# Optimization experiments

Hardware: AMD Instinct MI355X
Metric: run time of the kernel (lower is better)

## Reference

```python
import jax, jax.numpy as jnp
import numpy as np

B, S, H = 64, 512, 1024  # batch, seq_len, hidden (input_size == hidden_size per source)


def setup_inputs() -> dict:
    key = jax.random.key(0)
    k1, k2 = jax.random.split(key)
    x = jax.random.normal(k1, (B, S, H), dtype=jnp.float32)
    # xavier_uniform_ for U: bound = sqrt(6/(fan_in+fan_out))
    bound = float(np.sqrt(6.0 / (H + 4 * H)))
    U = jax.random.uniform(k2, (H, 4 * H), dtype=jnp.float32, minval=-bound, maxval=bound)
    bias = jnp.zeros((4 * H,), dtype=jnp.float32)
    return {"x": x, "U": U, "bias": bias}


def reference(x, U, bias):
    # Faithful LSTM recurrence (peephole=False; note: W is declared in the
    # original module but never used in forward, and the gate matmul uses U
    # on the input x_t, exactly as in the source).
    batch = x.shape[0]
    HS = U.shape[0]
    h0 = jnp.zeros((batch, HS), dtype=x.dtype)
    c0 = jnp.zeros((batch, HS), dtype=x.dtype)

    def step(carry, x_t):
        h_t, c_t = carry
        gates = x_t @ U + bias  # [B, 4H]
        i_t = jax.nn.sigmoid(gates[:, :HS])
        f_t = jax.nn.sigmoid(gates[:, HS:2 * HS])
        g_t = jnp.tanh(gates[:, 2 * HS:3 * HS])
        o_t = jax.nn.sigmoid(gates[:, 3 * HS:])
        c_t = f_t * c_t + i_t * g_t
        h_t = o_t * jnp.tanh(c_t)
        return (h_t, c_t), h_t

    (h_T, c_T), hs = jax.lax.scan(step, (h0, c0), jnp.swapaxes(x, 0, 1))  # hs: [S, B, H]
    hidden_sequence = jnp.swapaxes(hs, 0, 1)  # [B, S, H]
    return hidden_sequence, (h_T, c_T)
```

## Files before the change

### kernel.cpp

```cpp
#include <hip/hip_runtime.h>
#include <hip/hip_bf16.h>
#include <stdint.h>

typedef __bf16 bf16x8 __attribute__((ext_vector_type(8)));
typedef float  f32x4  __attribute__((ext_vector_type(4)));
typedef unsigned short u16x8 __attribute__((ext_vector_type(8)));
typedef unsigned short u16x4 __attribute__((ext_vector_type(4)));
typedef _Float16 f16x4 __attribute__((ext_vector_type(4)));

#define HS    1024
#define FOURH 4096
#define SEQ   512
#define BATCH 64

#define BAR()  asm volatile("s_barrier" ::: "memory")
#define VMW(n) asm volatile("s_waitcnt vmcnt(" #n ")" ::: "memory")

__device__ __forceinline__ unsigned short f2bf(float f) {
    unsigned u = __builtin_bit_cast(unsigned, f);
    u = (u + 0x7FFFu + ((u >> 16) & 1u)) >> 16;
    return (unsigned short)u;
}

__device__ __forceinline__ void gload_lds16(const void* g, void* l) {
    __builtin_amdgcn_global_load_lds(
        (const __attribute__((address_space(1))) void*)g,
        (__attribute__((address_space(3))) void*)l, 16, 0, 0);
}

__device__ __forceinline__ float fsigmoid(float v) {
    return __builtin_amdgcn_rcpf(1.f + __expf(-v));
}
__device__ __forceinline__ float ftanh(float v) {
    return 1.f - 2.f * __builtin_amdgcn_rcpf(1.f + __expf(2.f * v));
}

__global__ __launch_bounds__(256) void convert_x(const float* __restrict__ x,
                                                 unsigned short* __restrict__ xb,
                                                 long n8) {
    long i = (long)blockIdx.x * blockDim.x + threadIdx.x;
    long stride = (long)gridDim.x * blockDim.x;
    for (; i < n8; i += stride) {
        const float4* p = (const float4*)(x + i * 8);
        float4 a = p[0], b = p[1];
        u16x8 o;
        o[0] = f2bf(a.x); o[1] = f2bf(a.y); o[2] = f2bf(a.z); o[3] = f2bf(a.w);
        o[4] = f2bf(b.x); o[5] = f2bf(b.y); o[6] = f2bf(b.z); o[7] = f2bf(b.w);
        *(u16x8*)(xb + i * 8) = o;
    }
}

__global__ __launch_bounds__(256) void transpose_u(const float* __restrict__ U,
                                                   unsigned short* __restrict__ Ut) {
    __shared__ float tile[32][33];
    int bx = blockIdx.x;
    int tn = bx >> 5;
    int tk = bx & 31;
    int c = threadIdx.x & 31;
    int r = threadIdx.x >> 5;
#pragma unroll
    for (int i = 0; i < 4; ++i) {
        int k = tk * 32 + r + i * 8;
        tile[r + i * 8][c] = U[(size_t)k * FOURH + tn * 32 + c];
    }
    __syncthreads();
#pragma unroll
    for (int i = 0; i < 4; ++i) {
        int nl = r + i * 8;
        Ut[(size_t)(tn * 32 + nl) * HS + tk * 32 + c] = f2bf(tile[c][nl]);
    }
}

__global__ __launch_bounds__(512, 1) void gemm_gates8(
    const unsigned short* __restrict__ Xb,
    const unsigned short* __restrict__ Ut,
    const float* __restrict__ bias,
    _Float16* __restrict__ gates,
    int lg2chunk, int s0) {
    __shared__ unsigned short LDSU[65536];

    int nwg = gridDim.x;
    int bid = blockIdx.x;
    int wg = (bid & 7) * (nwg >> 3) + (bid >> 3);
    int mt = wg >> 4;
    int nt = wg & 15;

    int tid = threadIdx.x;
    int w = tid >> 6, l = tid & 63;
    int wr = w >> 2, wc = w & 3;
    int lr = l & 15, lg = l >> 4;

    const int m0 = mt * 256, n0 = nt * 256;
    const int cmask = (1 << lg2chunk) - 1;

    const int rdo = lr * 32 + ((lg * 8) ^ ((lr & 8) << 1));

    const int srow = l >> 2;
    const int skin = ((l & 3) * 8) ^ (((l >> 5) & 1) << 4);

    const unsigned short* pAq[4];
    const unsigned short* pBq[4];
#pragma unroll
    for (int q = 0; q < 4; ++q) {
        int rowg = q * 64 + (w >> 1) * 16 + srow;
        int mrow = m0 + rowg;
        int b = mrow >> lg2chunk, sl2 = mrow & cmask;
        pAq[q] = Xb + (size_t)(b * SEQ + s0 + sl2) * HS + (w & 1) * 32 + skin;
        pBq[q] = Ut + (size_t)(n0 + rowg) * HS + (w & 1) * 32 + skin;
    }
    const int dsub = (w >> 1) * 2 + (w & 1);

    f32x4 acc[8][4];
#pragma unroll
    for (int mi = 0; mi < 8; ++mi)
#pragma unroll
        for (int ni = 0; ni < 4; ++ni) acc[mi][ni] = 0.f;

#define SA(T, Q) gload_lds16(pAq[Q] + (T) * 64, \
        &LDSU[(((T) & 1) << 15) + ((Q) * 8 + dsub) * 512])
#define SB(T, Q) gload_lds16(pBq[Q] + (T) * 64, \
        &LDSU[(((T) & 1) << 15) + 16384 + ((Q) * 8 + dsub) * 512])

    bf16x8 aq[2][4], bn0[2][2], bn1[2][2];

#define RDA(MH) \
    _Pragma("unroll") for (int ks = 0; ks < 2; ++ks) \
    _Pragma("unroll") for (int mi = 0; mi < 4; ++mi) \
        aq[ks][mi] = *(const bf16x8*)(buf + ((wr * 8 + (MH) * 4 + mi) * 2 + ks) * 512 + rdo)
#define RDB(NH, BN) \
    _Pragma("unroll") for (int ks = 0; ks < 2; ++ks) \
    _Pragma("unroll") for (int ni = 0; ni < 2; ++ni) \
        BN[ks][ni] = *(const bf16x8*)(buf + 16384 + ((wc * 4 + (NH) * 2 + ni) * 2 + ks) * 512 + rdo)
#define MMQ(MH, NH, BN) \
    __builtin_amdgcn_s_setprio(1); \
    _Pragma("unroll") for (int ks = 0; ks < 2; ++ks) \
    _Pragma("unroll") for (int mi = 0; mi < 4; ++mi) \
    _Pragma("unroll") for (int ni = 0; ni < 2; ++ni) \
        acc[(MH) * 4 + mi][(NH) * 2 + ni] = __builtin_amdgcn_mfma_f32_16x16x32_bf16( \
            aq[ks][mi], BN[ks][ni], acc[(MH) * 4 + mi][(NH) * 2 + ni], 0, 0, 0); \
    __builtin_amdgcn_s_setprio(0)

    SA(0, 0); SA(0, 2); SB(0, 0); SB(0, 1); SB(0, 2); SB(0, 3); SA(0, 1); SA(0, 3);
    VMW(2); BAR();

    for (int t = 0; t < 16; ++t) {
        const unsigned short* buf = &LDSU[(t & 1) << 15];
        RDA(0);
        RDB(0, bn0);
        if (t < 15) { SA(t + 1, 0); SA(t + 1, 2); }
        MMQ(0, 0, bn0);
        RDB(1, bn1);
        if (t < 15) { SB(t + 1, 0); SB(t + 1, 1); SB(t + 1, 2); SB(t + 1, 3); }
        MMQ(0, 1, bn1);
        if (t < 15) { VMW(6); } else { VMW(0); }
        BAR();
        RDA(1);
        if (t < 15) { SA(t + 1, 1); SA(t + 1, 3); }
        MMQ(1, 1, bn1);
        MMQ(1, 0, bn0);
        if (t < 15) { VMW(2); }
        BAR();
    }

#pragma unroll
    for (int ni = 0; ni < 4; ++ni) {
        int gcol = n0 + wc * 64 + ni * 16 + lr;
        bool is_g = ((gcol >> 10) == 2);
        float bv = bias[gcol];
#pragma unroll
        for (int mi = 0; mi < 8; ++mi) {
            int rg = ((m0 + wr * 128 + mi * 16) >> 2) + lg;
            u16x4 pk;
#pragma unroll
            for (int r = 0; r < 4; ++r) {
                float v = acc[mi][ni][r] + bv;
                float e = is_g ? ftanh(v) : fsigmoid(v);
                pk[r] = __builtin_bit_cast(unsigned short, (_Float16)e);
            }
            *(u16x4*)(gates + ((size_t)rg * FOURH + gcol) * 4) = pk;
        }
    }
#undef SA
#undef SB
#undef RDA
#undef RDB
#undef MMQ
}

__global__ __launch_bounds__(256) void lstm_recur(
    const _Float16* __restrict__ gates,
    float* __restrict__ out,
    float* __restrict__ cstate,
    int chunk, int s0) {
    int t = blockIdx.x * 256 + threadIdx.x;
    int b = t >> 10, h = t & 1023;
    float c = (s0 == 0) ? 0.f : cstate[t];
    const _Float16* gp = gates + ((size_t)((b * chunk) >> 2) * FOURH + h) * 4;
    float* op = out + (size_t)(b * SEQ + s0) * HS + h;
    float hv = 0.f;
    const int ng = chunk >> 2;
    for (int g4 = 0; g4 < ng; g4 += 2) {
        f16x4 iv[2], fv[2], gv[2], ov[2];
#pragma unroll
        for (int u = 0; u < 2; ++u) {
            const _Float16* q = gp + (size_t)(g4 + u) * (FOURH * 4);
            iv[u] = *(const f16x4*)(q);
            fv[u] = *(const f16x4*)(q + 4096);
            gv[u] = *(const f16x4*)(q + 8192);
            ov[u] = *(const f16x4*)(q + 12288);
        }
#pragma unroll
        for (int u = 0; u < 2; ++u) {
#pragma unroll
            for (int r = 0; r < 4; ++r) {
                c = (float)fv[u][r] * c + (float)iv[u][r] * (float)gv[u][r];
                float th = ftanh(c);
                hv = (float)ov[u][r] * th;
                op[(size_t)((g4 + u) * 4 + r) * HS] = hv;
            }
        }
    }
    cstate[t] = c;
    if (s0 + chunk == SEQ) {
        out[(size_t)BATCH * SEQ * HS + t] = hv;
        out[(size_t)BATCH * SEQ * HS + BATCH * HS + t] = c;
    }
}

extern "C" void kernel_launch(void* const* d_in, const int* in_sizes, int n_in,
                              void* d_out, int out_size, void* d_ws, size_t ws_size,
                              hipStream_t stream) {
    const float* x    = (const float*)d_in[0];
    const float* U    = (const float*)d_in[1];
    const float* bias = (const float*)d_in[2];
    float* out = (float*)d_out;
    char*  ws  = (char*)d_ws;

    unsigned short* Xb = (unsigned short*)ws;
    unsigned short* Ut = (unsigned short*)(ws + 67108864);
    float* cstate      = (float*)(ws + 75497472);
    _Float16* gates    = (_Float16*)(ws + 75759616);
    const size_t fixed = 75759616;

    int chunk = 512;
    while (chunk > 4 && fixed + (size_t)BATCH * chunk * FOURH * 2 > ws_size)
        chunk >>= 1;
    int lg2 = 31 - __builtin_clz(chunk);

    convert_x<<<2048, 256, 0, stream>>>(x, Xb, (long)BATCH * SEQ * HS / 8);
    transpose_u<<<4096, 256, 0, stream>>>(U, Ut);

    for (int s0 = 0; s0 < SEQ; s0 += chunk) {
        int mtiles = (BATCH * chunk) / 256;
        gemm_gates8<<<mtiles * 16, 512, 0, stream>>>(Xb, Ut, bias, gates, lg2, s0);
        lstm_recur<<<256, 256, 0, stream>>>(gates, out, cstate, chunk, s0);
    }
}
```

Baseline: 401.3 us.

## Switch gate GEMM from 16x16x32 to 32x32x16 MFMA with matching LDS layout

Rewrites the input-projection GEMM to use the 32x32x16 bf16 MFMA instead of 16x16x32. The LDS staging layout, swizzle, global-to-LDS load mapping and epilogue indexing are all reorganized to match the 32x32 fragment shape. Each wave now issues fewer, larger MFMAs and does fewer LDS reads per FLOP. It uses 16-wide accumulators and changes the load/compute interleave, which could affect register pressure and bank conflicts.

```diff
diff --git a/kernel.cpp b/kernel.cpp
--- a/kernel.cpp
+++ b/kernel.cpp
@@ -3,7 +3,7 @@
 #include <stdint.h>
 
 typedef __bf16 bf16x8 __attribute__((ext_vector_type(8)));
-typedef float  f32x4  __attribute__((ext_vector_type(4)));
+typedef float  f32x16 __attribute__((ext_vector_type(16)));
 typedef unsigned short u16x8 __attribute__((ext_vector_type(8)));
 typedef unsigned short u16x4 __attribute__((ext_vector_type(4)));
 typedef _Float16 f16x4 __attribute__((ext_vector_type(4)));
@@ -88,100 +88,104 @@
     int tid = threadIdx.x;
     int w = tid >> 6, l = tid & 63;
     int wr = w >> 2, wc = w & 3;
-    int lr = l & 15, lg = l >> 4;
+    int l31 = l & 31, lhi = l >> 5;
 
     const int m0 = mt * 256, n0 = nt * 256;
     const int cmask = (1 << lg2chunk) - 1;
 
-    const int rdo = lr * 32 + ((lg * 8) ^ ((lr & 8) << 1));
-
-    const int srow = l >> 2;
-    const int skin = ((l & 3) * 8) ^ (((l >> 5) & 1) << 4);
-
-    const unsigned short* pAq[4];
-    const unsigned short* pBq[4];
-#pragma unroll
-    for (int q = 0; q < 4; ++q) {
-        int rowg = q * 64 + (w >> 1) * 16 + srow;
-        int mrow = m0 + rowg;
+    const int ro = l31 * 16 + ((lhi ^ ((l31 >> 2) & 1)) << 3);
+
+    const int k8src = ((l & 1) ^ ((l >> 3) & 1)) * 8;
+
+    const int msR1 = (w >> 1) + ((w >> 2) << 1);
+    const int msR2 = msR1 + 2;
+    const int ksw = (w & 1);
+
+    auto mkA = [&](int ms) {
+        int mrow = m0 + ms * 32 + (l >> 1);
         int b = mrow >> lg2chunk, sl2 = mrow & cmask;
-        pAq[q] = Xb + (size_t)(b * SEQ + s0 + sl2) * HS + (w & 1) * 32 + skin;
-        pBq[q] = Ut + (size_t)(n0 + rowg) * HS + (w & 1) * 32 + skin;
-    }
-    const int dsub = (w >> 1) * 2 + (w & 1);
-
-    f32x4 acc[8][4];
-#pragma unroll
-    for (int mi = 0; mi < 8; ++mi)
-#pragma unroll
-        for (int ni = 0; ni < 4; ++ni) acc[mi][ni] = 0.f;
-
-#define SA(T, Q) gload_lds16(pAq[Q] + (T) * 64, \
-        &LDSU[(((T) & 1) << 15) + ((Q) * 8 + dsub) * 512])
-#define SB(T, Q) gload_lds16(pBq[Q] + (T) * 64, \
-        &LDSU[(((T) & 1) << 15) + 16384 + ((Q) * 8 + dsub) * 512])
-
-    bf16x8 aq[2][4], bn0[2][2], bn1[2][2];
+        return Xb + (size_t)(b * SEQ + s0 + sl2) * HS + k8src;
+    };
+    const unsigned short* pA1 = mkA(msR1);
+    const unsigned short* pA2 = mkA(msR2);
+    const unsigned short* pB  = Ut + (size_t)(n0 + w * 32 + (l >> 1)) * HS + k8src;
+
+    f32x16 acc[4][2];
+#pragma unroll
+    for (int mi = 0; mi < 4; ++mi)
+#pragma unroll
+        for (int ni = 0; ni < 2; ++ni) acc[mi][ni] = 0.f;
+
+#define SA1(T, S) gload_lds16(pA1 + (T) * 64 + (ksw + 2 * (S)) * 16, \
+        &LDSU[(((T) & 1) << 15) + (msR1 * 4 + ksw + 2 * (S)) * 512])
+#define SA2(T, S) gload_lds16(pA2 + (T) * 64 + (ksw + 2 * (S)) * 16, \
+        &LDSU[(((T) & 1) << 15) + (msR2 * 4 + ksw + 2 * (S)) * 512])
+#define SBS(T, S) gload_lds16(pB + (T) * 64 + (S) * 16, \
+        &LDSU[(((T) & 1) << 15) + 16384 + (w * 4 + (S)) * 512])
+
+    bf16x8 av[2][4], bv_[2][4];
 
 #define RDA(MH) \
-    _Pragma("unroll") for (int ks = 0; ks < 2; ++ks) \
-    _Pragma("unroll") for (int mi = 0; mi < 4; ++mi) \
-        aq[ks][mi] = *(const bf16x8*)(buf + ((wr * 8 + (MH) * 4 + mi) * 2 + ks) * 512 + rdo)
-#define RDB(NH, BN) \
-    _Pragma("unroll") for (int ks = 0; ks < 2; ++ks) \
+    _Pragma("unroll") for (int ks = 0; ks < 4; ++ks) \
+    _Pragma("unroll") for (int mi = 0; mi < 2; ++mi) \
+        av[mi][ks] = *(const bf16x8*)(buf + ((wr * 4 + (MH) * 2 + mi) * 4 + ks) * 512 + ro)
+#define RDB() \
+    _Pragma("unroll") for (int ks = 0; ks < 4; ++ks) \
     _Pragma("unroll") for (int ni = 0; ni < 2; ++ni) \
-        BN[ks][ni] = *(const bf16x8*)(buf + 16384 + ((wc * 4 + (NH) * 2 + ni) * 2 + ks) * 512 + rdo)
-#define MMQ(MH, NH, BN) \
+        bv_[ni][ks] = *(const bf16x8*)(buf + 16384 + ((wc * 2 + ni) * 4 + ks) * 512 + ro)
+#define MMQ(MH) \
     __builtin_amdgcn_s_setprio(1); \
-    _Pragma("unroll") for (int ks = 0; ks < 2; ++ks) \
-    _Pragma("unroll") for (int mi = 0; mi < 4; ++mi) \
+    _Pragma("unroll") for (int ks = 0; ks < 4; ++ks) \
+    _Pragma("unroll") for (int mi = 0; mi < 2; ++mi) \
     _Pragma("unroll") for (int ni = 0; ni < 2; ++ni) \
-        acc[(MH) * 4 + mi][(NH) * 2 + ni] = __builtin_amdgcn_mfma_f32_16x16x32_bf16( \
-            aq[ks][mi], BN[ks][ni], acc[(MH) * 4 + mi][(NH) * 2 + ni], 0, 0, 0); \
+        acc[(MH) * 2 + mi][ni] = __builtin_amdgcn_mfma_f32_32x32x16_bf16( \
+            av[mi][ks], bv_[ni][ks], acc[(MH) * 2 + mi][ni], 0, 0, 0); \
     __builtin_amdgcn_s_setprio(0)
 
-    SA(0, 0); SA(0, 2); SB(0, 0); SB(0, 1); SB(0, 2); SB(0, 3); SA(0, 1); SA(0, 3);
+    SA1(0, 0); SA1(0, 1); SBS(0, 0); SBS(0, 1); SBS(0, 2); SBS(0, 3);
+    SA2(0, 0); SA2(0, 1);
     VMW(2); BAR();
 
     for (int t = 0; t < 16; ++t) {
         const unsigned short* buf = &LDSU[(t & 1) << 15];
         RDA(0);
-        RDB(0, bn0);
-        if (t < 15) { SA(t + 1, 0); SA(t + 1, 2); }
-        MMQ(0, 0, bn0);
-        RDB(1, bn1);
-        if (t < 15) { SB(t + 1, 0); SB(t + 1, 1); SB(t + 1, 2); SB(t + 1, 3); }
-        MMQ(0, 1, bn1);
+        RDB();
+        if (t < 15) { SA1(t + 1, 0); SA1(t + 1, 1);
+                      SBS(t + 1, 0); SBS(t + 1, 1); SBS(t + 1, 2); SBS(t + 1, 3); }
+        MMQ(0);
         if (t < 15) { VMW(6); } else { VMW(0); }
         BAR();
         RDA(1);
-        if (t < 15) { SA(t + 1, 1); SA(t + 1, 3); }
-        MMQ(1, 1, bn1);
-        MMQ(1, 0, bn0);
+        if (t < 15) { SA2(t + 1, 0); SA2(t + 1, 1); }
+        MMQ(1);
         if (t < 15) { VMW(2); }
         BAR();
     }
 
 #pragma unroll
-    for (int ni = 0; ni < 4; ++ni) {
-        int gcol = n0 + wc * 64 + ni * 16 + lr;
+    for (int ni = 0; ni < 2; ++ni) {
+        int gcol = n0 + wc * 64 + ni * 32 + l31;
         bool is_g = ((gcol >> 10) == 2);
         float bv = bias[gcol];
 #pragma unroll
-        for (int mi = 0; mi < 8; ++mi) {
-            int rg = ((m0 + wr * 128 + mi * 16) >> 2) + lg;
-            u16x4 pk;
-#pragma unroll
-            for (int r = 0; r < 4; ++r) {
-                float v = acc[mi][ni][r] + bv;
-                float e = is_g ? ftanh(v) : fsigmoid(v);
-                pk[r] = __builtin_bit_cast(unsigned short, (_Float16)e);
+        for (int mi = 0; mi < 4; ++mi) {
+            int rgb = ((m0 + wr * 128 + mi * 32) >> 2) + lhi;
+#pragma unroll
+            for (int j = 0; j < 4; ++j) {
+                u16x4 pk;
+#pragma unroll
+                for (int r = 0; r < 4; ++r) {
+                    float v = acc[mi][ni][j * 4 + r] + bv;
+                    float e = is_g ? ftanh(v) : fsigmoid(v);
+                    pk[r] = __builtin_bit_cast(unsigned short, (_Float16)e);
+                }
+                *(u16x4*)(gates + ((size_t)(rgb + 2 * j) * FOURH + gcol) * 4) = pk;
             }
-            *(u16x4*)(gates + ((size_t)rg * FOURH + gcol) * 4) = pk;
         }
     }
-#undef SA
-#undef SB
+#undef SA1
+#undef SA2
+#undef SBS
 #undef RDA
 #undef RDB
 #undef MMQ
```

Measured after the change: 438.2 us. 9.2% more time.

## Reschedule gate GEMM main loop into fine-grained half-tile prefetch pipeline

Applied to the files above, without the earlier changes.

The bf16 gate GEMM main loop now splits A and B tile loads into low and high halves and prefetches B and the low half of A two k-steps ahead, while the high half of A is fetched one step ahead. Barriers and lgkmcnt waits are interleaved between each MFMA quarter, so LDS reuse of the double buffer is staged per half. The aim is to hide more global-to-LDS latency behind MFMA work. The cost is many more barriers per iteration, and a more fragile buffer-reuse ordering.

```diff
diff --git a/kernel.cpp b/kernel.cpp
--- a/kernel.cpp
+++ b/kernel.cpp
@@ -15,6 +15,7 @@
 
 #define BAR()  asm volatile("s_barrier" ::: "memory")
 #define VMW(n) asm volatile("s_waitcnt vmcnt(" #n ")" ::: "memory")
+#define LGKM0() asm volatile("s_waitcnt lgkmcnt(0)" ::: "memory")
 
 __device__ __forceinline__ unsigned short f2bf(float f) {
     unsigned u = __builtin_bit_cast(unsigned, f);
@@ -99,16 +100,28 @@
     const int skin = ((l & 3) * 8) ^ (((l >> 5) & 1) << 4);
 
     const unsigned short* pAq[4];
-    const unsigned short* pBq[4];
 #pragma unroll
     for (int q = 0; q < 4; ++q) {
         int rowg = q * 64 + (w >> 1) * 16 + srow;
         int mrow = m0 + rowg;
         int b = mrow >> lg2chunk, sl2 = mrow & cmask;
         pAq[q] = Xb + (size_t)(b * SEQ + s0 + sl2) * HS + (w & 1) * 32 + skin;
-        pBq[q] = Ut + (size_t)(n0 + rowg) * HS + (w & 1) * 32 + skin;
     }
     const int dsub = (w >> 1) * 2 + (w & 1);
+
+    const unsigned short* pBL[2];
+    const unsigned short* pBH[2];
+    int slBL[2], slBH[2];
+#pragma unroll
+    for (int j = 0; j < 2; ++j) {
+        int idx = 4 * j + (w >> 1);
+        int rbL = ((idx >> 1) << 2) + (idx & 1);
+        int rbH = rbL + 2;
+        pBL[j] = Ut + (size_t)(n0 + rbL * 16 + srow) * HS + (w & 1) * 32 + skin;
+        pBH[j] = Ut + (size_t)(n0 + rbH * 16 + srow) * HS + (w & 1) * 32 + skin;
+        slBL[j] = rbL * 2 + (w & 1);
+        slBH[j] = rbH * 2 + (w & 1);
+    }
 
     f32x4 acc[8][4];
 #pragma unroll
@@ -118,8 +131,16 @@
 
 #define SA(T, Q) gload_lds16(pAq[Q] + (T) * 64, \
         &LDSU[(((T) & 1) << 15) + ((Q) * 8 + dsub) * 512])
-#define SB(T, Q) gload_lds16(pBq[Q] + (T) * 64, \
-        &LDSU[(((T) & 1) << 15) + 16384 + ((Q) * 8 + dsub) * 512])
+#define SALO(T) { SA(T, 0); SA(T, 2); }
+#define SAHI(T) { SA(T, 1); SA(T, 3); }
+#define SBLO(T) { gload_lds16(pBL[0] + (T) * 64, \
+        &LDSU[(((T) & 1) << 15) + 16384 + slBL[0] * 512]); \
+                  gload_lds16(pBL[1] + (T) * 64, \
+        &LDSU[(((T) & 1) << 15) + 16384 + slBL[1] * 512]); }
+#define SBHI(T) { gload_lds16(pBH[0] + (T) * 64, \
+        &LDSU[(((T) & 1) << 15) + 16384 + slBH[0] * 512]); \
+                  gload_lds16(pBH[1] + (T) * 64, \
+        &LDSU[(((T) & 1) << 15) + 16384 + slBH[1] * 512]); }
 
     bf16x8 aq[2][4], bn0[2][2], bn1[2][2];
 
@@ -140,25 +161,33 @@
             aq[ks][mi], BN[ks][ni], acc[(MH) * 4 + mi][(NH) * 2 + ni], 0, 0, 0); \
     __builtin_amdgcn_s_setprio(0)
 
-    SA(0, 0); SA(0, 2); SB(0, 0); SB(0, 1); SB(0, 2); SB(0, 3); SA(0, 1); SA(0, 3);
-    VMW(2); BAR();
+    SALO(0); SBLO(0); SBHI(0); SAHI(0);
+    SALO(1); SBLO(1); SBHI(1);
+    VMW(6); BAR();
 
     for (int t = 0; t < 16; ++t) {
         const unsigned short* buf = &LDSU[(t & 1) << 15];
         RDA(0);
         RDB(0, bn0);
-        if (t < 15) { SA(t + 1, 0); SA(t + 1, 2); }
+        if (t < 15) SAHI(t + 1);
+        asm volatile("s_waitcnt lgkmcnt(8)" ::: "memory");
+        BAR(); LGKM0();
         MMQ(0, 0, bn0);
+        BAR();
         RDB(1, bn1);
-        if (t < 15) { SB(t + 1, 0); SB(t + 1, 1); SB(t + 1, 2); SB(t + 1, 3); }
+        if (t < 14) SALO(t + 2);
+        BAR(); LGKM0();
         MMQ(0, 1, bn1);
-        if (t < 15) { VMW(6); } else { VMW(0); }
         BAR();
         RDA(1);
-        if (t < 15) { SA(t + 1, 1); SA(t + 1, 3); }
+        if (t < 14) SBLO(t + 2);
+        BAR(); LGKM0();
         MMQ(1, 1, bn1);
+        BAR();
+        if (t < 14) SBHI(t + 2);
+        BAR();
         MMQ(1, 0, bn0);
-        if (t < 15) { VMW(2); }
+        if (t < 14) { VMW(6); } else if (t == 14) { VMW(0); }
         BAR();
     }
 
@@ -181,7 +210,10 @@
         }
     }
 #undef SA
-#undef SB
+#undef SALO
+#undef SAHI
+#undef SBLO
+#undef SBHI
 #undef RDA
 #undef RDB
 #undef MMQ
```

Result: no change. 406.8 us (+1.4%).

## Shrink GEMM tile to 256x128 with K=32 triple-buffered LDS pipeline

Applied to the files above, without the earlier changes.

Rewrites the gate GEMM to use 256x128 output tiles with K steps of 32, triple-buffered in LDS (72KB instead of 128KB), and raises the occupancy hint to allow more workgroups per CU. The grid doubles along N. The aim is to hide memory latency through higher occupancy and a deeper prefetch pipeline. In exchange, the smaller N tile reduces operand reuse per block and the loop needs twice as many barriers.

```diff
diff --git a/kernel.cpp b/kernel.cpp
--- a/kernel.cpp
+++ b/kernel.cpp
@@ -71,26 +71,26 @@
     }
 }
 
-__global__ __launch_bounds__(512, 1) void gemm_gates8(
+__global__ __launch_bounds__(512, 4) void gemm_gates8(
     const unsigned short* __restrict__ Xb,
     const unsigned short* __restrict__ Ut,
     const float* __restrict__ bias,
     _Float16* __restrict__ gates,
     int lg2chunk, int s0) {
-    __shared__ unsigned short LDSU[65536];
+    __shared__ unsigned short LDSU[36864];
 
     int nwg = gridDim.x;
     int bid = blockIdx.x;
     int wg = (bid & 7) * (nwg >> 3) + (bid >> 3);
-    int mt = wg >> 4;
-    int nt = wg & 15;
+    int mt = wg >> 5;
+    int nt = wg & 31;
 
     int tid = threadIdx.x;
     int w = tid >> 6, l = tid & 63;
-    int wr = w >> 2, wc = w & 3;
+    int wr = w >> 1, wc = w & 1;
     int lr = l & 15, lg = l >> 4;
 
-    const int m0 = mt * 256, n0 = nt * 256;
+    const int m0 = mt * 256, n0 = nt * 128;
     const int cmask = (1 << lg2chunk) - 1;
 
     const int rdo = lr * 32 + ((lg * 8) ^ ((lr & 8) << 1));
@@ -98,93 +98,79 @@
     const int srow = l >> 2;
     const int skin = ((l & 3) * 8) ^ (((l >> 5) & 1) << 4);
 
-    const unsigned short* pAq[4];
-    const unsigned short* pBq[4];
-#pragma unroll
-    for (int q = 0; q < 4; ++q) {
-        int rowg = q * 64 + (w >> 1) * 16 + srow;
-        int mrow = m0 + rowg;
-        int b = mrow >> lg2chunk, sl2 = mrow & cmask;
-        pAq[q] = Xb + (size_t)(b * SEQ + s0 + sl2) * HS + (w & 1) * 32 + skin;
-        pBq[q] = Ut + (size_t)(n0 + rowg) * HS + (w & 1) * 32 + skin;
-    }
-    const int dsub = (w >> 1) * 2 + (w & 1);
-
-    f32x4 acc[8][4];
-#pragma unroll
-    for (int mi = 0; mi < 8; ++mi)
+    const unsigned short* pA0;
+    const unsigned short* pA1;
+    const unsigned short* pB;
+    {
+        int r1 = m0 + (2 * w) * 16 + srow;
+        int b1 = r1 >> lg2chunk, q1 = r1 & cmask;
+        pA0 = Xb + (size_t)(b1 * SEQ + s0 + q1) * HS + skin;
+        int r2 = m0 + (2 * w + 1) * 16 + srow;
+        int b2 = r2 >> lg2chunk, q2 = r2 & cmask;
+        pA1 = Xb + (size_t)(b2 * SEQ + s0 + q2) * HS + skin;
+        pB  = Ut + (size_t)(n0 + w * 16 + srow) * HS + skin;
+    }
+
+    f32x4 acc[4][4];
+#pragma unroll
+    for (int mi = 0; mi < 4; ++mi)
 #pragma unroll
         for (int ni = 0; ni < 4; ++ni) acc[mi][ni] = 0.f;
 
-#define SA(T, Q) gload_lds16(pAq[Q] + (T) * 64, \
-        &LDSU[(((T) & 1) << 15) + ((Q) * 8 + dsub) * 512])
-#define SB(T, Q) gload_lds16(pBq[Q] + (T) * 64, \
-        &LDSU[(((T) & 1) << 15) + 16384 + ((Q) * 8 + dsub) * 512])
-
-    bf16x8 aq[2][4], bn0[2][2], bn1[2][2];
-
-#define RDA(MH) \
-    _Pragma("unroll") for (int ks = 0; ks < 2; ++ks) \
-    _Pragma("unroll") for (int mi = 0; mi < 4; ++mi) \
-        aq[ks][mi] = *(const bf16x8*)(buf + ((wr * 8 + (MH) * 4 + mi) * 2 + ks) * 512 + rdo)
-#define RDB(NH, BN) \
-    _Pragma("unroll") for (int ks = 0; ks < 2; ++ks) \
-    _Pragma("unroll") for (int ni = 0; ni < 2; ++ni) \
-        BN[ks][ni] = *(const bf16x8*)(buf + 16384 + ((wc * 4 + (NH) * 2 + ni) * 2 + ks) * 512 + rdo)
-#define MMQ(MH, NH, BN) \
-    __builtin_amdgcn_s_setprio(1); \
-    _Pragma("unroll") for (int ks = 0; ks < 2; ++ks) \
-    _Pragma("unroll") for (int mi = 0; mi < 4; ++mi) \
-    _Pragma("unroll") for (int ni = 0; ni < 2; ++ni) \
-        acc[(MH) * 4 + mi][(NH) * 2 + ni] = __builtin_amdgcn_mfma_f32_16x16x32_bf16( \
-            aq[ks][mi], BN[ks][ni], acc[(MH) * 4 + mi][(NH) * 2 + ni], 0, 0, 0); \
-    __builtin_amdgcn_s_setprio(0)
-
-    SA(0, 0); SA(0, 2); SB(0, 0); SB(0, 1); SB(0, 2); SB(0, 3); SA(0, 1); SA(0, 3);
-    VMW(2); BAR();
-
-    for (int t = 0; t < 16; ++t) {
-        const unsigned short* buf = &LDSU[(t & 1) << 15];
-        RDA(0);
-        RDB(0, bn0);
-        if (t < 15) { SA(t + 1, 0); SA(t + 1, 2); }
-        MMQ(0, 0, bn0);
-        RDB(1, bn1);
-        if (t < 15) { SB(t + 1, 0); SB(t + 1, 1); SB(t + 1, 2); SB(t + 1, 3); }
-        MMQ(0, 1, bn1);
-        if (t < 15) { VMW(6); } else { VMW(0); }
-        BAR();
-        RDA(1);
-        if (t < 15) { SA(t + 1, 1); SA(t + 1, 3); }
-        MMQ(1, 1, bn1);
-        MMQ(1, 0, bn0);
-        if (t < 15) { VMW(2); }
-        BAR();
-    }
+#define STG(T, dst) { \
+    gload_lds16(pA0 + (T) * 32, (dst) + (2 * w) * 512); \
+    gload_lds16(pA1 + (T) * 32, (dst) + (2 * w + 1) * 512); \
+    gload_lds16(pB  + (T) * 32, (dst) + 8192 + w * 512); }
+
+    unsigned short* b0 = &LDSU[0];
+    unsigned short* b1 = &LDSU[12288];
+    unsigned short* b2 = &LDSU[24576];
+
+    STG(0, b0); STG(1, b1);
+    VMW(3); BAR();
+
+    bf16x8 av[4], bv[4];
+    for (int t = 0; t < 32; ++t) {
+#pragma unroll
+        for (int mi = 0; mi < 4; ++mi)
+            av[mi] = *(const bf16x8*)(b0 + (wr * 4 + mi) * 512 + rdo);
+#pragma unroll
+        for (int ni = 0; ni < 4; ++ni)
+            bv[ni] = *(const bf16x8*)(b0 + 8192 + (wc * 4 + ni) * 512 + rdo);
+        if (t < 30) STG(t + 2, b2);
+        __builtin_amdgcn_s_setprio(1);
+#pragma unroll
+        for (int mi = 0; mi < 4; ++mi)
+#pragma unroll
+            for (int ni = 0; ni < 4; ++ni)
+                acc[mi][ni] = __builtin_amdgcn_mfma_f32_16x16x32_bf16(
+                    av[mi], bv[ni], acc[mi][ni], 0, 0, 0);
+        __builtin_amdgcn_s_setprio(0);
+        if (t < 30)      { VMW(3); }
+        else if (t == 30){ VMW(0); }
+        if (t < 31) BAR();
+        unsigned short* tmp = b0; b0 = b1; b1 = b2; b2 = tmp;
+    }
+#undef STG
 
 #pragma unroll
     for (int ni = 0; ni < 4; ++ni) {
         int gcol = n0 + wc * 64 + ni * 16 + lr;
         bool is_g = ((gcol >> 10) == 2);
-        float bv = bias[gcol];
-#pragma unroll
-        for (int mi = 0; mi < 8; ++mi) {
-            int rg = ((m0 + wr * 128 + mi * 16) >> 2) + lg;
+        float bv2 = bias[gcol];
+#pragma unroll
+        for (int mi = 0; mi < 4; ++mi) {
+            int rg = ((m0 + wr * 64 + mi * 16) >> 2) + lg;
             u16x4 pk;
 #pragma unroll
             for (int r = 0; r < 4; ++r) {
-                float v = acc[mi][ni][r] + bv;
+                float v = acc[mi][ni][r] + bv2;
                 float e = is_g ? ftanh(v) : fsigmoid(v);
                 pk[r] = __builtin_bit_cast(unsigned short, (_Float16)e);
             }
             *(u16x4*)(gates + ((size_t)rg * FOURH + gcol) * 4) = pk;
         }
     }
-#undef SA
-#undef SB
-#undef RDA
-#undef RDB
-#undef MMQ
 }
 
 __global__ __launch_bounds__(256) void lstm_recur(
@@ -252,7 +238,7 @@
 
     for (int s0 = 0; s0 < SEQ; s0 += chunk) {
         int mtiles = (BATCH * chunk) / 256;
-        gemm_gates8<<<mtiles * 16, 512, 0, stream>>>(Xb, Ut, bias, gates, lg2, s0);
+        gemm_gates8<<<mtiles * 32, 512, 0, stream>>>(Xb, Ut, bias, gates, lg2, s0);
         lstm_recur<<<256, 256, 0, stream>>>(gates, out, cstate, chunk, s0);
     }
 }
```

New measurement: 428.2 us. 1.07x slower.
